# Optimization experiments

Hardware: AMD Instinct MI355X
Metric: run time of the kernel (lower is better)

Reference implementation:

```python
import jax, jax.numpy as jnp
import numpy as np

ATT_HEAD, IN_DIM, OUT_DIM = 8, 768, 96
B, N = 8, 1024
LEAKY_ALPHA = 0.2


def setup_inputs() -> dict:
    key = jax.random.key(0)
    ks = jax.random.split(key, 8)
    feat_in = jax.random.normal(ks[0], (B, N, IN_DIM), dtype=jnp.float32)
    adj = jax.random.randint(ks[1], (B, N, N), 0, 2).astype(jnp.float32)
    # xavier-ish init scales
    W = jax.random.normal(ks[2], (ATT_HEAD, IN_DIM, OUT_DIM), dtype=jnp.float32) * (1.0 / np.sqrt(IN_DIM))
    b = jnp.zeros((OUT_DIM,), dtype=jnp.float32)
    w_src = jax.random.normal(ks[3], (ATT_HEAD, OUT_DIM, 1), dtype=jnp.float32) * (1.0 / np.sqrt(OUT_DIM))
    w_dst = jax.random.normal(ks[4], (ATT_HEAD, OUT_DIM, 1), dtype=jnp.float32) * (1.0 / np.sqrt(OUT_DIM))
    Hw = jax.random.normal(ks[5], (IN_DIM, IN_DIM), dtype=jnp.float32) * (1.0 / np.sqrt(IN_DIM))
    Hb = jnp.zeros((IN_DIM,), dtype=jnp.float32)
    return {"feat_in": feat_in, "adj": adj, "W": W, "b": b,
            "w_src": w_src, "w_dst": w_dst, "Hw": Hw, "Hb": Hb}


def reference(feat_in, adj, W, b, w_src, w_dst, Hw, Hb):
    batch, n, _ = feat_in.shape
    # per-head projection: [B,H,N,O]
    h = jnp.einsum('bni,hio->bhno', feat_in, W)
    t = jnp.tanh(h)
    a_src = jnp.einsum('bhno,hoq->bhnq', t, w_src)[..., 0]  # [B,H,N]
    a_dst = jnp.einsum('bhno,hoq->bhnq', t, w_dst)[..., 0]  # [B,H,N]
    attn = a_src[:, :, :, None] + a_dst[:, :, None, :]       # [B,H,N,N]
    attn = jnp.where(attn >= 0, attn, LEAKY_ALPHA * attn)
    mask = adj[:, None, :, :] == 0                            # 1-adj as bool
    attn = jnp.where(mask, jnp.float32(-999.0), attn)
    attn = jax.nn.softmax(attn, axis=-1)
    feat_out = jnp.einsum('bhnm,bhmo->bhno', attn, h) + b     # [B,H,N,O]
    feat_out = jnp.transpose(feat_out, (0, 2, 1, 3)).reshape(batch, n, -1)
    feat_out = jax.nn.elu(feat_out)
    gate = jax.nn.sigmoid(feat_in @ Hw.T + Hb)
    return gate * feat_out + (1.0 - gate) * feat_in
```

## Files before the change

### kernel.cpp

```cpp
#include <hip/hip_runtime.h>
#include <cstddef>

#define BATCH 8
#define NN 1024
#define IN_DIM 768
#define OUT_DIM 96
#define HEADS 8
#define M_ROWS 8192
#define NCOLS 1536

typedef __attribute__((ext_vector_type(8))) short short8;
typedef __attribute__((ext_vector_type(4))) float f32x4;
typedef __attribute__((ext_vector_type(4))) unsigned short ushort4v;

typedef __attribute__((address_space(1))) void gvoid_t;
typedef __attribute__((address_space(3))) void lvoid_t;

__device__ __forceinline__ void gload_lds16(const void* g, void* l) {
    __builtin_amdgcn_global_load_lds((gvoid_t*)(unsigned long long)g,
                                     (lvoid_t*)(unsigned int)(unsigned long long)l,
                                     16, 0, 0);
}

__device__ __forceinline__ unsigned short f2bf(float x) {
    unsigned int u = __builtin_bit_cast(unsigned int, x);
    u += 0x7fffu + ((u >> 16) & 1u);
    return (unsigned short)(u >> 16);
}
__device__ __forceinline__ float bf2f(unsigned short u) {
    unsigned int v = ((unsigned int)u) << 16;
    return __builtin_bit_cast(float, v);
}
__device__ __forceinline__ float tanh_fast(float x) {
    return 1.f - 2.f / (__expf(2.f * x) + 1.f);
}

__global__ void xb_kernel(const float* __restrict__ x, unsigned short* __restrict__ xb) {
    int idx = blockIdx.x * 256 + threadIdx.x;
    const float4* p = (const float4*)(x + (size_t)idx * 8);
    float4 a = p[0], b = p[1];
    short8 r;
    r[0] = (short)f2bf(a.x); r[1] = (short)f2bf(a.y); r[2] = (short)f2bf(a.z); r[3] = (short)f2bf(a.w);
    r[4] = (short)f2bf(b.x); r[5] = (short)f2bf(b.y); r[6] = (short)f2bf(b.z); r[7] = (short)f2bf(b.w);
    *(short8*)(xb + (size_t)idx * 8) = r;
}

__global__ void pack_w_kernel(const float* __restrict__ W, unsigned short* __restrict__ BT) {
    int idx = blockIdx.x * 256 + threadIdx.x;
    int c = idx / IN_DIM, i = idx % IN_DIM;
    int h = c / OUT_DIM, o = c % OUT_DIM;
    BT[(size_t)c * IN_DIM + i] = f2bf(W[((size_t)h * IN_DIM + i) * OUT_DIM + o]);
}
__global__ void pack_hw_kernel(const float* __restrict__ Hw, unsigned short* __restrict__ BT) {
    int idx = blockIdx.x * 256 + threadIdx.x;
    int c = idx / IN_DIM, i = idx % IN_DIM;
    BT[(size_t)(768 + c) * IN_DIM + i] = f2bf(Hw[(size_t)c * IN_DIM + i]);
}

__global__ void pack_abits_kernel(const float* __restrict__ adj, unsigned int* __restrict__ abits) {
    int idx = blockIdx.x * 256 + threadIdx.x;
    const float4* p = (const float4*)(adj + (size_t)idx * 32);
    unsigned int m = 0;
    #pragma unroll
    for (int q = 0; q < 8; ++q) {
        float4 v = p[q];
        m |= (v.x != 0.f ? 1u : 0u) << (q * 4 + 0);
        m |= (v.y != 0.f ? 1u : 0u) << (q * 4 + 1);
        m |= (v.z != 0.f ? 1u : 0u) << (q * 4 + 2);
        m |= (v.w != 0.f ? 1u : 0u) << (q * 4 + 3);
    }
    abits[idx] = m;
}

__global__ __launch_bounds__(256) void gemm1_kernel(
        const unsigned short* __restrict__ Xb, const unsigned short* __restrict__ BT,
        unsigned short* __restrict__ h_bt, float* __restrict__ glog) {
    __shared__ __align__(16) unsigned short As[128 * 64];
    __shared__ __align__(16) unsigned short Bs[128 * 64];
    int m0 = blockIdx.x * 128;
    int c0 = blockIdx.y * 128;
    int t = threadIdx.x;
    int w = t >> 6, lane = t & 63, l15 = t & 15, quad = lane >> 4;
    f32x4 acc[2][8] = {};
    for (int k0 = 0; k0 < IN_DIM; k0 += 64) {
        __syncthreads();
        #pragma unroll
        for (int cc = 0; cc < 4; ++cc) {
            int base64 = (w * 4 + cc) * 64;
            int p = base64 + lane;
            int r = p >> 3, qs = p & 7;
            int qb = qs ^ (r & 7);
            gload_lds16(Xb + (size_t)(m0 + r) * IN_DIM + k0 + qb * 8, As + base64 * 8);
            gload_lds16(BT + (size_t)(c0 + r) * IN_DIM + k0 + qb * 8, Bs + base64 * 8);
        }
        __syncthreads();
        #pragma unroll
        for (int ks = 0; ks < 2; ++ks) {
            short8 af[2], bfr[8];
            #pragma unroll
            for (int mt = 0; mt < 2; ++mt) {
                int r = w * 32 + mt * 16 + l15;
                int cb = (ks * 4 + quad) ^ (r & 7);
                af[mt] = *(const short8*)(As + r * 64 + cb * 8);
            }
            #pragma unroll
            for (int nt = 0; nt < 8; ++nt) {
                int r = nt * 16 + l15;
                int cb = (ks * 4 + quad) ^ (r & 7);
                bfr[nt] = *(const short8*)(Bs + r * 64 + cb * 8);
            }
            #pragma unroll
            for (int mt = 0; mt < 2; ++mt)
                #pragma unroll
                for (int nt = 0; nt < 8; ++nt)
                    acc[mt][nt] = __builtin_amdgcn_mfma_f32_16x16x32_bf16(af[mt], bfr[nt], acc[mt][nt], 0, 0, 0);
        }
    }
    int b = m0 >> 10;
    #pragma unroll
    for (int mt = 0; mt < 2; ++mt) {
        int rowbase = m0 + w * 32 + mt * 16 + quad * 4;
        int nbase = rowbase & 1023;
        #pragma unroll
        for (int nt = 0; nt < 8; ++nt) {
            int c = c0 + nt * 16 + l15;
            if (c < 768) {
                int hh = c / OUT_DIM, o = c % OUT_DIM;
                ushort4v hb;
                hb[0] = f2bf(acc[mt][nt][0]); hb[1] = f2bf(acc[mt][nt][1]);
                hb[2] = f2bf(acc[mt][nt][2]); hb[3] = f2bf(acc[mt][nt][3]);
                *(ushort4v*)(h_bt + ((size_t)(b * 8 + hh) * OUT_DIM + o) * NN + nbase) = hb;
            } else {
                int cg = c - 768;
                #pragma unroll
                for (int reg = 0; reg < 4; ++reg)
                    glog[(size_t)(rowbase + reg) * 768 + cg] = acc[mt][nt][reg];
            }
        }
    }
}

__global__ __launch_bounds__(256) void a_kernel(const unsigned short* __restrict__ h_bt,
                                                const float* __restrict__ w_src,
                                                const float* __restrict__ w_dst,
                                                float* __restrict__ a_src, float* __restrict__ a_dst) {
    __shared__ unsigned short ht[96 * 72];
    __shared__ float ws_s[96], wd_s[96];
    __shared__ float pps[4][64], ppd[4][64];
    int bh = blockIdx.x >> 4;
    int n0 = (blockIdx.x & 15) * 64;
    int head = bh & 7;
    int t = threadIdx.x;
    if (t < 96) { ws_s[t] = w_src[head * 96 + t]; wd_s[t] = w_dst[head * 96 + t]; }
    for (int f = t; f < 768; f += 256) {
        int row = f >> 3, c8 = (f & 7) * 8;
        *(short8*)(ht + row * 72 + c8) = *(const short8*)(h_bt + ((size_t)bh * 96 + row) * NN + n0 + c8);
    }
    __syncthreads();
    int n = t & 63, part = t >> 6;
    float ps = 0.f, pd = 0.f;
    #pragma unroll
    for (int oo = 0; oo < 24; ++oo) {
        int o = part * 24 + oo;
        float th = tanh_fast(bf2f(ht[o * 72 + n]));
        ps += th * ws_s[o];
        pd += th * wd_s[o];
    }
    pps[part][n] = ps; ppd[part][n] = pd;
    __syncthreads();
    if (t < 64) {
        float s = pps[0][t] + pps[1][t] + pps[2][t] + pps[3][t];
        float d = ppd[0][t] + ppd[1][t] + ppd[2][t] + ppd[3][t];
        a_src[bh * 1024 + n0 + t] = s * 1.44269504f;
        a_dst[bh * 1024 + n0 + t] = d * 1.44269504f;
    }
}

__global__ __launch_bounds__(256) void attn_kernel(
        const unsigned short* __restrict__ h_bt, const unsigned int* __restrict__ abits,
        const float* __restrict__ a_src_g, const float* __restrict__ a_dst_g,
        const float* __restrict__ glog, const float* __restrict__ feat_in,
        const float* __restrict__ bias, const float* __restrict__ Hb,
        float* __restrict__ out) {
    __shared__ __align__(16) unsigned short es[64 * 72];
    __shared__ __align__(16) unsigned short hs[96 * 72];
    __shared__ __align__(16) float adst[1024];
    __shared__ __align__(16) float asrc[64];
    __shared__ float bias_s[96], hb_s[96];
    int blk = blockIdx.x;
    int bh = blk >> 4, i0 = (blk & 15) * 64, b = bh >> 3, hh = bh & 7;
    int t = threadIdx.x;
    int w = t >> 6, lane = t & 63, l15 = t & 15, quad = lane >> 4;
    for (int q = 0; q < 4; ++q) adst[q * 256 + t] = a_dst_g[bh * 1024 + q * 256 + t];
    if (t < 64) asrc[t] = a_src_g[bh * 1024 + i0 + t];
    if (t >= 64 && t < 160) { bias_s[t - 64] = bias[t - 64]; hb_s[t - 64] = Hb[hh * 96 + t - 64]; }
    const unsigned short* hhp = h_bt + (size_t)bh * 96 * NN;
    int il = t >> 2, jq = (t & 3) * 16;
    const unsigned int* ab_row = abits + ((size_t)b * NN + i0 + il) * 32;
    short8 hreg[3];
    #pragma unroll
    for (int q = 0; q < 3; ++q) {
        int f = t + q * 256;
        int row = f >> 3, c8 = (f & 7) * 8;
        hreg[q] = *(const short8*)(hhp + (size_t)row * NN + c8);
    }
    unsigned int mword = ab_row[jq >> 5];
    f32x4 acc[7] = {};
    short8 ones = {};
    if (l15 == 0) {
        #pragma unroll
        for (int u = 0; u < 8; ++u) ones[u] = (short)0x3F80;
    }
    __syncthreads();
    float si = asrc[il];
    for (int j0 = 0; j0 < 1024; j0 += 64) {
        #pragma unroll
        for (int q = 0; q < 3; ++q) {
            int f = t + q * 256;
            int row = f >> 3, c8 = (f & 7) * 8;
            *(short8*)(hs + row * 72 + c8) = hreg[q];
        }
        unsigned int m16 = (mword >> (jq & 16)) & 0xFFFFu;
        f32x4 dv[4];
        #pragma unroll
        for (int q = 0; q < 4; ++q) dv[q] = *(const f32x4*)(&adst[j0 + jq + q * 4]);
        float ev[16];
        #pragma unroll
        for (int u = 0; u < 16; ++u) {
            float s = si + dv[u >> 2][u & 3];
            float l = fmaxf(s, 0.2f * s);
            float e = __builtin_amdgcn_exp2f(l);
            ev[u] = ((m16 >> u) & 1u) ? e : 0.f;
        }
        union { unsigned int u[8]; short8 s8[2]; } pk;
        #pragma unroll
        for (int p = 0; p < 8; ++p) {
            unsigned int u0 = __builtin_bit_cast(unsigned int, ev[2 * p]) + 0x8000u;
            unsigned int u1 = __builtin_bit_cast(unsigned int, ev[2 * p + 1]) + 0x8000u;
            pk.u[p] = __builtin_amdgcn_perm(u1, u0, 0x07060302);
        }
        *(short8*)(es + il * 72 + jq) = pk.s8[0];
        *(short8*)(es + il * 72 + jq + 8) = pk.s8[1];
        int jn = j0 + 64;
        if (jn < 1024) {
            #pragma unroll
            for (int q = 0; q < 3; ++q) {
                int f = t + q * 256;
                int row = f >> 3, c8 = (f & 7) * 8;
                hreg[q] = *(const short8*)(hhp + (size_t)row * NN + jn + c8);
            }
            mword = ab_row[(jn + jq) >> 5];
        }
        __syncthreads();
        #pragma unroll
        for (int ks = 0; ks < 2; ++ks) {
            short8 af = *(const short8*)(es + (w * 16 + l15) * 72 + ks * 32 + quad * 8);
            #pragma unroll
            for (int nt = 0; nt < 6; ++nt) {
                short8 bfr = *(const short8*)(hs + (nt * 16 + l15) * 72 + ks * 32 + quad * 8);
                acc[nt] = __builtin_amdgcn_mfma_f32_16x16x32_bf16(af, bfr, acc[nt], 0, 0, 0);
            }
            acc[6] = __builtin_amdgcn_mfma_f32_16x16x32_bf16(af, ones, acc[6], 0, 0, 0);
        }
        __syncthreads();
    }
    int rowq = i0 + w * 16 + quad * 4;
    #pragma unroll
    for (int reg = 0; reg < 4; ++reg) {
        float ssum = __shfl(acc[6][reg], (lane & 48));
        float inv = (ssum > 0.f) ? 1.f / ssum : 0.f;
        int n = rowq + reg;
        size_t mrow = ((size_t)b * NN + n) * 768 + hh * 96;
        #pragma unroll
        for (int nt = 0; nt < 6; ++nt) {
            int cl = nt * 16 + l15;
            float fo = acc[nt][reg] * inv + bias_s[cl];
            float e = (fo > 0.f) ? fo : (__expf(fo) - 1.f);
            float z = glog[mrow + cl] + hb_s[cl];
            float g = 1.f / (1.f + __expf(-z));
            float x = feat_in[mrow + cl];
            out[mrow + cl] = g * e + (1.f - g) * x;
        }
    }
}

extern "C" void kernel_launch(void* const* d_in, const int* in_sizes, int n_in,
                              void* d_out, int out_size, void* d_ws, size_t ws_size,
                              hipStream_t stream) {
    const float* feat_in = (const float*)d_in[0];
    const float* adj     = (const float*)d_in[1];
    const float* W       = (const float*)d_in[2];
    const float* bbias   = (const float*)d_in[3];
    const float* w_src   = (const float*)d_in[4];
    const float* w_dst   = (const float*)d_in[5];
    const float* Hw      = (const float*)d_in[6];
    const float* Hb      = (const float*)d_in[7];
    float* out = (float*)d_out;
    char* base = (char*)d_ws;

    unsigned short* Xb    = (unsigned short*)(base);
    unsigned short* BcatT = (unsigned short*)(base + 12582912);
    unsigned short* h_bt  = (unsigned short*)(base + 14942208);
    float* glog  = (float*)(base + 27525120);
    float* a_src = (float*)(base + 52690944);
    float* a_dst = (float*)(base + 52953088);
    unsigned int* abits = (unsigned int*)(base);

    xb_kernel<<<(M_ROWS * IN_DIM / 8) / 256, 256, 0, stream>>>(feat_in, Xb);
    pack_w_kernel<<<(768 * IN_DIM) / 256, 256, 0, stream>>>(W, BcatT);
    pack_hw_kernel<<<(768 * IN_DIM) / 256, 256, 0, stream>>>(Hw, BcatT);
    gemm1_kernel<<<dim3(M_ROWS / 128, NCOLS / 128), 256, 0, stream>>>(Xb, BcatT, h_bt, glog);
    pack_abits_kernel<<<(BATCH * NN * NN / 32) / 256, 256, 0, stream>>>(adj, abits);
    a_kernel<<<64 * 16, 256, 0, stream>>>(h_bt, w_src, w_dst, a_src, a_dst);
    attn_kernel<<<64 * 16, 256, 0, stream>>>(h_bt, abits, a_src, a_dst, glog, feat_in, bbias, Hb, out);
}
```

Baseline: 195.9 us.

## Fuse gate sigmoid into GEMM epilogue, read adj directly, double-buffer h tiles

Drops the adjacency bit-packing kernel; the attention kernel now reads float adjacency rows straight into registers in the MFMA A-fragment layout, which removes the shared-memory staging for the exp tile. The gate bias and sigmoid move into the GEMM epilogue and the gate is stored as fp16, halving that intermediate. The attention epilogue reads the bf16 copy of feat_in instead of fp32. h tiles are double-buffered through LDS with swizzled async global-to-LDS loads. The cost is that each of the 8 heads now rereads the full fp32 adjacency (8x more adj traffic than the bitmask), and the output blend uses bf16 features and an fp16 gate, which lowers precision.

After: 201.0 us. 1.03x slower.

```diff
diff --git a/kernel.cpp b/kernel.cpp
--- a/kernel.cpp
+++ b/kernel.cpp
@@ -57,30 +57,18 @@
     BT[(size_t)(768 + c) * IN_DIM + i] = f2bf(Hw[(size_t)c * IN_DIM + i]);
 }
 
-__global__ void pack_abits_kernel(const float* __restrict__ adj, unsigned int* __restrict__ abits) {
-    int idx = blockIdx.x * 256 + threadIdx.x;
-    const float4* p = (const float4*)(adj + (size_t)idx * 32);
-    unsigned int m = 0;
-    #pragma unroll
-    for (int q = 0; q < 8; ++q) {
-        float4 v = p[q];
-        m |= (v.x != 0.f ? 1u : 0u) << (q * 4 + 0);
-        m |= (v.y != 0.f ? 1u : 0u) << (q * 4 + 1);
-        m |= (v.z != 0.f ? 1u : 0u) << (q * 4 + 2);
-        m |= (v.w != 0.f ? 1u : 0u) << (q * 4 + 3);
-    }
-    abits[idx] = m;
-}
-
 __global__ __launch_bounds__(256) void gemm1_kernel(
         const unsigned short* __restrict__ Xb, const unsigned short* __restrict__ BT,
-        unsigned short* __restrict__ h_bt, float* __restrict__ glog) {
+        const float* __restrict__ Hb,
+        unsigned short* __restrict__ h_bt, unsigned short* __restrict__ gate) {
     __shared__ __align__(16) unsigned short As[128 * 64];
     __shared__ __align__(16) unsigned short Bs[128 * 64];
+    __shared__ float hbs[128];
     int m0 = blockIdx.x * 128;
     int c0 = blockIdx.y * 128;
     int t = threadIdx.x;
     int w = t >> 6, lane = t & 63, l15 = t & 15, quad = lane >> 4;
+    if (c0 >= 768 && t < 128) hbs[t] = Hb[c0 - 768 + t];
     f32x4 acc[2][8] = {};
     for (int k0 = 0; k0 < IN_DIM; k0 += 64) {
         __syncthreads();
@@ -131,10 +119,15 @@
                 hb[2] = f2bf(acc[mt][nt][2]); hb[3] = f2bf(acc[mt][nt][3]);
                 *(ushort4v*)(h_bt + ((size_t)(b * 8 + hh) * OUT_DIM + o) * NN + nbase) = hb;
             } else {
+                int cl = nt * 16 + l15;
                 int cg = c - 768;
                 #pragma unroll
-                for (int reg = 0; reg < 4; ++reg)
-                    glog[(size_t)(rowbase + reg) * 768 + cg] = acc[mt][nt][reg];
+                for (int reg = 0; reg < 4; ++reg) {
+                    float z = acc[mt][nt][reg] + hbs[cl];
+                    float g = __builtin_amdgcn_rcpf(1.f + __builtin_amdgcn_exp2f(-1.44269504f * z));
+                    _Float16 gh = (_Float16)g;
+                    gate[(size_t)(rowbase + reg) * 768 + cg] = __builtin_bit_cast(unsigned short, gh);
+                }
             }
         }
     }
@@ -177,34 +170,37 @@
 }
 
 __global__ __launch_bounds__(256) void attn_kernel(
-        const unsigned short* __restrict__ h_bt, const unsigned int* __restrict__ abits,
+        const unsigned short* __restrict__ h_bt, const float* __restrict__ adj,
         const float* __restrict__ a_src_g, const float* __restrict__ a_dst_g,
-        const float* __restrict__ glog, const float* __restrict__ feat_in,
-        const float* __restrict__ bias, const float* __restrict__ Hb,
-        float* __restrict__ out) {
-    __shared__ __align__(16) unsigned short es[64 * 72];
-    __shared__ __align__(16) unsigned short hs[96 * 72];
+        const unsigned short* __restrict__ gate, const unsigned short* __restrict__ Xb,
+        const float* __restrict__ bias, float* __restrict__ out) {
+    __shared__ __align__(16) unsigned short hs[2][96 * 64];
     __shared__ __align__(16) float adst[1024];
-    __shared__ __align__(16) float asrc[64];
-    __shared__ float bias_s[96], hb_s[96];
+    __shared__ float asrc[64];
+    __shared__ float bias_s[96];
     int blk = blockIdx.x;
     int bh = blk >> 4, i0 = (blk & 15) * 64, b = bh >> 3, hh = bh & 7;
     int t = threadIdx.x;
     int w = t >> 6, lane = t & 63, l15 = t & 15, quad = lane >> 4;
     for (int q = 0; q < 4; ++q) adst[q * 256 + t] = a_dst_g[bh * 1024 + q * 256 + t];
-    if (t < 64) asrc[t] = a_src_g[bh * 1024 + i0 + t];
-    if (t >= 64 && t < 160) { bias_s[t - 64] = bias[t - 64]; hb_s[t - 64] = Hb[hh * 96 + t - 64]; }
+    if (t < 96) bias_s[t] = bias[t];
+    if (t >= 128 && t < 192) asrc[t - 128] = a_src_g[bh * 1024 + i0 + (t - 128)];
     const unsigned short* hhp = h_bt + (size_t)bh * 96 * NN;
-    int il = t >> 2, jq = (t & 3) * 16;
-    const unsigned int* ab_row = abits + ((size_t)b * NN + i0 + il) * 32;
-    short8 hreg[3];
-    #pragma unroll
-    for (int q = 0; q < 3; ++q) {
-        int f = t + q * 256;
-        int row = f >> 3, c8 = (f & 7) * 8;
-        hreg[q] = *(const short8*)(hhp + (size_t)row * NN + c8);
-    }
-    unsigned int mword = ab_row[jq >> 5];
+    #pragma unroll
+    for (int cc = 0; cc < 3; ++cc) {
+        int u0 = (w * 3 + cc) * 64;
+        int p = u0 + lane;
+        int r = p >> 3, qs = p & 7, qb = qs ^ (r & 7);
+        gload_lds16(hhp + (size_t)r * NN + qb * 8, (char*)&hs[0][0] + (size_t)u0 * 16);
+    }
+    int irow = i0 + w * 16 + l15;
+    const float* arow = adj + ((size_t)b * NN + irow) * NN;
+    float4 adjreg[4];
+    #pragma unroll
+    for (int ks = 0; ks < 2; ++ks) {
+        adjreg[2 * ks]     = *(const float4*)(arow + ks * 32 + quad * 8);
+        adjreg[2 * ks + 1] = *(const float4*)(arow + ks * 32 + quad * 8 + 4);
+    }
     f32x4 acc[7] = {};
     short8 ones = {};
     if (l15 == 0) {
@@ -212,55 +208,61 @@
         for (int u = 0; u < 8; ++u) ones[u] = (short)0x3F80;
     }
     __syncthreads();
-    float si = asrc[il];
+    float si = asrc[w * 16 + l15];
     for (int j0 = 0; j0 < 1024; j0 += 64) {
-        #pragma unroll
-        for (int q = 0; q < 3; ++q) {
-            int f = t + q * 256;
-            int row = f >> 3, c8 = (f & 7) * 8;
-            *(short8*)(hs + row * 72 + c8) = hreg[q];
-        }
-        unsigned int m16 = (mword >> (jq & 16)) & 0xFFFFu;
-        f32x4 dv[4];
-        #pragma unroll
-        for (int q = 0; q < 4; ++q) dv[q] = *(const f32x4*)(&adst[j0 + jq + q * 4]);
-        float ev[16];
-        #pragma unroll
-        for (int u = 0; u < 16; ++u) {
-            float s = si + dv[u >> 2][u & 3];
-            float l = fmaxf(s, 0.2f * s);
-            float e = __builtin_amdgcn_exp2f(l);
-            ev[u] = ((m16 >> u) & 1u) ? e : 0.f;
-        }
-        union { unsigned int u[8]; short8 s8[2]; } pk;
-        #pragma unroll
-        for (int p = 0; p < 8; ++p) {
-            unsigned int u0 = __builtin_bit_cast(unsigned int, ev[2 * p]) + 0x8000u;
-            unsigned int u1 = __builtin_bit_cast(unsigned int, ev[2 * p + 1]) + 0x8000u;
-            pk.u[p] = __builtin_amdgcn_perm(u1, u0, 0x07060302);
-        }
-        *(short8*)(es + il * 72 + jq) = pk.s8[0];
-        *(short8*)(es + il * 72 + jq + 8) = pk.s8[1];
+        int cur = (j0 >> 6) & 1;
         int jn = j0 + 64;
         if (jn < 1024) {
             #pragma unroll
-            for (int q = 0; q < 3; ++q) {
-                int f = t + q * 256;
-                int row = f >> 3, c8 = (f & 7) * 8;
-                hreg[q] = *(const short8*)(hhp + (size_t)row * NN + jn + c8);
-            }
-            mword = ab_row[(jn + jq) >> 5];
-        }
-        __syncthreads();
+            for (int cc = 0; cc < 3; ++cc) {
+                int u0 = (w * 3 + cc) * 64;
+                int p = u0 + lane;
+                int r = p >> 3, qs = p & 7, qb = qs ^ (r & 7);
+                gload_lds16(hhp + (size_t)r * NN + jn + qb * 8, (char*)&hs[cur ^ 1][0] + (size_t)u0 * 16);
+            }
+        }
+        short8 af[2];
         #pragma unroll
         for (int ks = 0; ks < 2; ++ks) {
-            short8 af = *(const short8*)(es + (w * 16 + l15) * 72 + ks * 32 + quad * 8);
+            f32x4 d0 = *(const f32x4*)(&adst[j0 + ks * 32 + quad * 8]);
+            f32x4 d1 = *(const f32x4*)(&adst[j0 + ks * 32 + quad * 8 + 4]);
+            float av[8] = {adjreg[2 * ks].x, adjreg[2 * ks].y, adjreg[2 * ks].z, adjreg[2 * ks].w,
+                           adjreg[2 * ks + 1].x, adjreg[2 * ks + 1].y, adjreg[2 * ks + 1].z, adjreg[2 * ks + 1].w};
+            float dv[8] = {d0[0], d0[1], d0[2], d0[3], d1[0], d1[1], d1[2], d1[3]};
+            float ev[8];
+            #pragma unroll
+            for (int u = 0; u < 8; ++u) {
+                float s = si + dv[u];
+                float l = fmaxf(s, 0.2f * s);
+                float e = __builtin_amdgcn_exp2f(l);
+                ev[u] = (av[u] != 0.f) ? e : 0.f;
+            }
+            union { unsigned int u4[4]; short8 s8; } pk;
+            #pragma unroll
+            for (int p2 = 0; p2 < 4; ++p2) {
+                unsigned int u0b = __builtin_bit_cast(unsigned int, ev[2 * p2]) + 0x8000u;
+                unsigned int u1b = __builtin_bit_cast(unsigned int, ev[2 * p2 + 1]) + 0x8000u;
+                pk.u4[p2] = __builtin_amdgcn_perm(u1b, u0b, 0x07060302);
+            }
+            af[ks] = pk.s8;
+        }
+        if (jn < 1024) {
+            #pragma unroll
+            for (int ks = 0; ks < 2; ++ks) {
+                adjreg[2 * ks]     = *(const float4*)(arow + jn + ks * 32 + quad * 8);
+                adjreg[2 * ks + 1] = *(const float4*)(arow + jn + ks * 32 + quad * 8 + 4);
+            }
+        }
+        #pragma unroll
+        for (int ks = 0; ks < 2; ++ks) {
             #pragma unroll
             for (int nt = 0; nt < 6; ++nt) {
-                short8 bfr = *(const short8*)(hs + (nt * 16 + l15) * 72 + ks * 32 + quad * 8);
-                acc[nt] = __builtin_amdgcn_mfma_f32_16x16x32_bf16(af, bfr, acc[nt], 0, 0, 0);
-            }
-            acc[6] = __builtin_amdgcn_mfma_f32_16x16x32_bf16(af, ones, acc[6], 0, 0, 0);
+                int r = nt * 16 + l15;
+                int qs = (ks * 4 + quad) ^ (r & 7);
+                short8 bfr = *(const short8*)(&hs[cur][(size_t)(r * 8 + qs) * 8]);
+                acc[nt] = __builtin_amdgcn_mfma_f32_16x16x32_bf16(af[ks], bfr, acc[nt], 0, 0, 0);
+            }
+            acc[6] = __builtin_amdgcn_mfma_f32_16x16x32_bf16(af[ks], ones, acc[6], 0, 0, 0);
         }
         __syncthreads();
     }
@@ -268,18 +270,18 @@
     #pragma unroll
     for (int reg = 0; reg < 4; ++reg) {
         float ssum = __shfl(acc[6][reg], (lane & 48));
-        float inv = (ssum > 0.f) ? 1.f / ssum : 0.f;
+        float inv = (ssum > 0.f) ? __builtin_amdgcn_rcpf(ssum) : 0.f;
         int n = rowq + reg;
         size_t mrow = ((size_t)b * NN + n) * 768 + hh * 96;
         #pragma unroll
         for (int nt = 0; nt < 6; ++nt) {
             int cl = nt * 16 + l15;
-            float fo = acc[nt][reg] * inv + bias_s[cl];
-            float e = (fo > 0.f) ? fo : (__expf(fo) - 1.f);
-            float z = glog[mrow + cl] + hb_s[cl];
-            float g = 1.f / (1.f + __expf(-z));
-            float x = feat_in[mrow + cl];
-            out[mrow + cl] = g * e + (1.f - g) * x;
+            float v = acc[nt][reg] * inv + bias_s[cl];
+            float e = (v > 0.f) ? v : (__builtin_amdgcn_exp2f(v * 1.44269504f) - 1.f);
+            _Float16 gh = __builtin_bit_cast(_Float16, gate[mrow + cl]);
+            float g = (float)gh;
+            float x = bf2f(Xb[mrow + cl]);
+            out[mrow + cl] = x + g * (e - x);
         }
     }
 }
@@ -301,16 +303,14 @@
     unsigned short* Xb    = (unsigned short*)(base);
     unsigned short* BcatT = (unsigned short*)(base + 12582912);
     unsigned short* h_bt  = (unsigned short*)(base + 14942208);
-    float* glog  = (float*)(base + 27525120);
-    float* a_src = (float*)(base + 52690944);
-    float* a_dst = (float*)(base + 52953088);
-    unsigned int* abits = (unsigned int*)(base);
+    unsigned short* gate  = (unsigned short*)(base + 27525120);
+    float* a_src = (float*)(base + 40108032);
+    float* a_dst = (float*)(base + 40370176);
 
     xb_kernel<<<(M_ROWS * IN_DIM / 8) / 256, 256, 0, stream>>>(feat_in, Xb);
     pack_w_kernel<<<(768 * IN_DIM) / 256, 256, 0, stream>>>(W, BcatT);
     pack_hw_kernel<<<(768 * IN_DIM) / 256, 256, 0, stream>>>(Hw, BcatT);
-    gemm1_kernel<<<dim3(M_ROWS / 128, NCOLS / 128), 256, 0, stream>>>(Xb, BcatT, h_bt, glog);
-    pack_abits_kernel<<<(BATCH * NN * NN / 32) / 256, 256, 0, stream>>>(adj, abits);
+    gemm1_kernel<<<dim3(M_ROWS / 128, NCOLS / 128), 256, 0, stream>>>(Xb, BcatT, Hb, h_bt, gate);
     a_kernel<<<64 * 16, 256, 0, stream>>>(h_bt, w_src, w_dst, a_src, a_dst);
-    attn_kernel<<<64 * 16, 256, 0, stream>>>(h_bt, abits, a_src, a_dst, glog, feat_in, bbias, Hb, out);
-}
+    attn_kernel<<<64 * 16, 256, 0, stream>>>(h_bt, adj, a_src, a_dst, gate, Xb, bbias, out);
+}
```
